# Kernel tuning notes

Hardware: AMD Instinct MI355X
Metric: run time of the kernel (lower is better)

The kernel has to match this reference:

```python
import jax, jax.numpy as jnp
import numpy as np
import math

HEAD_DIM = 64           # d_model // n_heads // 2
N_HEADS = 8
LAMBDA_INIT = 0.8 - 0.6 * math.exp(-0.3 * 6)  # depth=6
EPS = 1e-5


def setup_inputs() -> dict:
    key = jax.random.key(0)
    ks = jax.random.split(key, 8)
    B, T, S = 2, 2048, 2048
    return {
        "queries": jax.random.normal(ks[0], (B, 2 * N_HEADS, T, HEAD_DIM), jnp.float32),
        "keys": jax.random.normal(ks[1], (B, 2 * N_HEADS, S, HEAD_DIM), jnp.float32),
        "values": jax.random.normal(ks[2], (B, N_HEADS, S, 2 * HEAD_DIM), jnp.float32),
        "lambda_q1": 0.02 * jax.random.normal(ks[3], (HEAD_DIM,), jnp.float32),
        "lambda_k1": 0.02 * jax.random.normal(ks[4], (HEAD_DIM,), jnp.float32),
        "lambda_q2": 0.02 * jax.random.normal(ks[5], (HEAD_DIM,), jnp.float32),
        "lambda_k2": 0.02 * jax.random.normal(ks[6], (HEAD_DIM,), jnp.float32),
        "subln_weight": jnp.ones((2 * HEAD_DIM,), jnp.float32),
        "tgt_len": 2048,
        "src_len": 2048,
        "attn_mask": jnp.zeros((1,), jnp.bool_),
    }


def reference(queries, keys, values, lambda_q1, lambda_k1, lambda_q2, lambda_k2,
              subln_weight, tgt_len, src_len, attn_mask):
    B = queries.shape[0]
    scaling = HEAD_DIM ** -0.5
    q = queries * scaling
    # [B, 2H, T, S]
    attn_w = jnp.einsum('bhtd,bhsd->bhts', q, keys)
    attn_w = jax.nn.softmax(attn_w.astype(jnp.float32), axis=-1).astype(queries.dtype)
    lam1 = jnp.exp(jnp.sum(lambda_q1 * lambda_k1))
    lam2 = jnp.exp(jnp.sum(lambda_q2 * lambda_k2))
    lam_full = lam1 - lam2 + LAMBDA_INIT
    attn_w = attn_w.reshape(B, N_HEADS, 2, tgt_len, src_len)
    attn_w = attn_w[:, :, 0] - lam_full * attn_w[:, :, 1]   # [B, H, T, S]
    attn = jnp.einsum('bhts,bhse->bhte', attn_w, values)    # [B, H, T, 2*HEAD_DIM]
    # RMSNorm over last dim
    normed = attn * jax.lax.rsqrt(jnp.mean(jnp.square(attn.astype(jnp.float32)), axis=-1, keepdims=True) + EPS).astype(attn.dtype)
    normed = normed * subln_weight
    out = normed * (1.0 - LAMBDA_INIT)
    out = out.transpose(0, 2, 1, 3).reshape(B, tgt_len, N_HEADS * 2 * HEAD_DIM)
    return out
```

## Files before the change

### kernel.cpp

```cpp
#include <hip/hip_runtime.h>
#include <math.h>


#define NT    2048
#define D     64
#define DV    128
#define TQ    64
#define TS    32
#define NROUND (NT / (2 * TS))

#define LAMBDA_INIT 0.70082066706704814f
#define OUT_SCALE   0.29917933293295186f
#define QSCALE      0.18033688011112042f

typedef __attribute__((ext_vector_type(8)))  short    short8;
typedef __attribute__((ext_vector_type(4)))  short    short4v;
typedef __attribute__((ext_vector_type(8)))  _Float16 half8;
typedef __attribute__((ext_vector_type(2)))  __fp16   fp16x2;
typedef __attribute__((ext_vector_type(4)))  float    f32x4;
typedef unsigned short u16;
typedef unsigned int   u32;

#define MFMAH(a, b, c)  __builtin_amdgcn_mfma_f32_16x16x32_f16(a, b, c, 0, 0, 0)
#define MFMA16(a, b, c) __builtin_amdgcn_mfma_f32_16x16x32_bf16(a, b, c, 0, 0, 0)

#if __has_builtin(__builtin_amdgcn_exp2f)
#define EXP2F(x) __builtin_amdgcn_exp2f(x)
#else
#define EXP2F(x) exp2f(x)
#endif

union Hu { half8 v; _Float16 e[8]; u16 s[8]; short8 sv; };

__device__ __forceinline__ u16 f2h(float x) {
    Hu u; u.e[0] = (_Float16)x; return u.s[0];
}

__device__ __forceinline__ void glds16(const u16* g, const u16* l) {
    __builtin_amdgcn_global_load_lds(
        (const __attribute__((address_space(1))) void*)g,
        (__attribute__((address_space(3))) void*)l, 16, 0, 0);
}

__global__ __launch_bounds__(256) void prep_kv(
    const float* __restrict__ Kg, const float* __restrict__ Vg,
    const float* __restrict__ lq1, const float* __restrict__ lk1,
    const float* __restrict__ lq2, const float* __restrict__ lk2,
    u16* __restrict__ Kf, u16* __restrict__ Vf, float* __restrict__ lamw)
{
    __shared__ u16 th[64 * 136];
    const int bid = blockIdx.x;
    const int t   = threadIdx.x;
    if (bid < 2048) {
        const int idx = (bid * 256 + t) * 8;
        const float4 a = *(const float4*)(Kg + idx);
        const float4 b = *(const float4*)(Kg + idx + 4);
        Hu H;
        H.e[0] = (_Float16)a.x; H.e[1] = (_Float16)a.y;
        H.e[2] = (_Float16)a.z; H.e[3] = (_Float16)a.w;
        H.e[4] = (_Float16)b.x; H.e[5] = (_Float16)b.y;
        H.e[6] = (_Float16)b.z; H.e[7] = (_Float16)b.w;
        *(short8*)(Kf + idx) = H.sv;
        return;
    }
    if (bid == 2048) {
        if (t == 0) {
            float t1 = 0.f, t2 = 0.f;
            for (int i = 0; i < D; ++i) {
                t1 = fmaf(lq1[i], lk1[i], t1);
                t2 = fmaf(lq2[i], lk2[i], t2);
            }
            lamw[0] = __expf(t1) - __expf(t2) + LAMBDA_INIT;
        }
        return;
    }
    const int i  = bid - 2049;
    const int bh = i >> 5;
    const int eb = (i >> 4) & 1;
    const int sb = i & 15;
    const size_t vbase = (size_t)bh * NT * DV + (size_t)sb * 128 * DV + eb * 64;
    {
        const int r0 = t >> 4;
        const int c4 = (t & 15) * 4;
        #pragma unroll
        for (int rr = 0; rr < 8; ++rr) {
            const int row = r0 + rr * 16;
            const float4 x = *(const float4*)(Vg + vbase + (size_t)row * DV + c4);
            th[(c4 + 0) * 136 + row] = f2h(x.x);
            th[(c4 + 1) * 136 + row] = f2h(x.y);
            th[(c4 + 2) * 136 + row] = f2h(x.z);
            th[(c4 + 3) * 136 + row] = f2h(x.w);
        }
    }
    __syncthreads();
    const int e  = t >> 2;
    const int g  = t & 3;
    const size_t orow = ((size_t)bh * DV + eb * 64 + e) * NT + sb * 128;
    #pragma unroll
    for (int c = 0; c < 4; ++c) {
        Hu o;
        #pragma unroll
        for (int j = 0; j < 8; ++j)
            o.s[j] = th[e * 136 + g * 32 + 4 * c + (j & 3) + 16 * (j >> 2)];
        *(short8*)(Vf + orow + g * 32 + c * 8) = o.sv;
    }
}

struct SmemF {
    union {
        short8 c[4096];
        struct {
            float epi[2][32][132];
            float lbuf[2][2][2][32];
        } e;
    };
};

__global__ __launch_bounds__(512, 4) void diffattn_mfma17(
    const float* __restrict__ Qg,
    const u16* __restrict__ Kf, const u16* __restrict__ Vf,
    const float* __restrict__ lamw,
    const float* __restrict__ Wg, float* __restrict__ Outg)
{
    __shared__ SmemF sm;

    const int tid    = threadIdx.x;
    const int wv     = tid >> 6;
    const int lane   = tid & 63;
    const int quad   = lane >> 4;
    const int lc     = lane & 15;
    const int stripe = wv & 1;
    const int hh     = (wv >> 1) & 1;
    const int ks     = wv >> 2;
    const int wig    = wv & 3;
    const int qt     = blockIdx.x;
    const int bh     = blockIdx.y;
    const int b      = bh >> 3, h = bh & 7;

    const int head2b = b * 16 + 2 * h;
    const int bh8    = b * 8 + h;
    const float lam  = lamw[0];

    half8 qf[2][2];
    {
        const size_t qhead = (size_t)(head2b + hh) * NT * D;
        #pragma unroll
        for (int nq = 0; nq < 2; ++nq) {
            const int row = qt * TQ + stripe * 32 + nq * 16 + lc;
            #pragma unroll
            for (int k0 = 0; k0 < 2; ++k0) {
                const int d0 = k0 * 32 + quad * 8;
                const float4 x = *(const float4*)(Qg + qhead + (size_t)row * D + d0);
                const float4 y = *(const float4*)(Qg + qhead + (size_t)row * D + d0 + 4);
                Hu q;
                q.e[0] = (_Float16)(x.x * QSCALE); q.e[1] = (_Float16)(x.y * QSCALE);
                q.e[2] = (_Float16)(x.z * QSCALE); q.e[3] = (_Float16)(x.w * QSCALE);
                q.e[4] = (_Float16)(y.x * QSCALE); q.e[5] = (_Float16)(y.y * QSCALE);
                q.e[6] = (_Float16)(y.z * QSCALE); q.e[7] = (_Float16)(y.w * QSCALE);
                qf[nq][k0] = q.v;
            }
        }
    }

    f32x4 O_[2][8];
    #pragma unroll
    for (int nq = 0; nq < 2; ++nq)
        #pragma unroll
        for (int nt = 0; nt < 8; ++nt) O_[nq][nt] = (f32x4){0.f, 0.f, 0.f, 0.f};
    float lacA[2] = {0.f, 0.f};
    float lacB[2] = {0.f, 0.f};

    u32 kSrc[2], vSrc[2];
    u32 kLds[2], vLds[2];
    #pragma unroll
    for (int t = 0; t < 2; ++t) {
        const int p   = (wig * 2 + t) * 64 + lane;
        const int hhs = p >> 8;
        const int n   = (p >> 3) & 31;
        const int db  = (p & 7) ^ (n & 7);
        kSrc[t] = (u32)(((head2b + hhs) * NT + n) * D + db * 8);
        kLds[t] = (u32)((ks * 512 + (wig * 2 + t) * 64) * 16);
        const int e = p >> 2;
        const int u = (p & 3) ^ ((e >> 1) & 3);
        vSrc[t] = (u32)((bh8 * DV + e) * NT + u * 8);
        vLds[t] = (u32)((1024 + ks * 512 + (wig * 2 + t) * 64) * 16);
    }
    const u16* ldsu = (const u16*)&sm.c[0];

    #pragma unroll
    for (int t = 0; t < 2; ++t) {
        glds16(Kf + kSrc[t] + (u32)ks * (TS * D), ldsu + (kLds[t] >> 1));
        glds16(Vf + vSrc[t] + (u32)ks * TS,       ldsu + (vLds[t] >> 1));
    }
    __syncthreads();

    u32 kOff[2][2];
    #pragma unroll
    for (int k0 = 0; k0 < 2; ++k0)
        #pragma unroll
        for (int mt = 0; mt < 2; ++mt)
            kOff[k0][mt] = (u32)((ks * 512 + hh * 256 + (mt * 16 + lc) * 8 +
                                  ((4 * k0 + quad) ^ (lc & 7))) * 8);
    u32 vOff[8];
    {
        const int swzv = quad ^ ((lc >> 1) & 3);
        #pragma unroll
        for (int nt = 0; nt < 8; ++nt)
            vOff[nt] = (u32)((1024 + ks * 512 + (nt * 16 + lc) * 4 + swzv) * 8);
    }

    const f32x4 z4 = {0.f, 0.f, 0.f, 0.f};

    for (int r = 0; r < NROUND; ++r) {
        const u32 bo = ((u32)(r & 1)) << 14;

        if (r < NROUND - 1) {
            const u32 tn = (u32)(2 * (r + 1) + ks);
            const u32 ab = ((u32)((r + 1) & 1)) << 14;
            #pragma unroll
            for (int t = 0; t < 2; ++t) {
                glds16(Kf + kSrc[t] + tn * (TS * D), ldsu + ab + (kLds[t] >> 1));
                glds16(Vf + vSrc[t] + tn * TS,       ldsu + ab + (vLds[t] >> 1));
            }
        }

        f32x4 sf[2][2];
        {
            const half8 k00 = *(const half8*)(ldsu + bo + kOff[0][0]);
            const half8 k01 = *(const half8*)(ldsu + bo + kOff[0][1]);
            sf[0][0] = MFMAH(k00, qf[0][0], z4);
            sf[0][1] = MFMAH(k00, qf[1][0], z4);
            sf[1][0] = MFMAH(k01, qf[0][0], z4);
            sf[1][1] = MFMAH(k01, qf[1][0], z4);
            const half8 k10 = *(const half8*)(ldsu + bo + kOff[1][0]);
            const half8 k11 = *(const half8*)(ldsu + bo + kOff[1][1]);
            sf[0][0] = MFMAH(k10, qf[0][1], sf[0][0]);
            sf[0][1] = MFMAH(k10, qf[1][1], sf[0][1]);
            sf[1][0] = MFMAH(k11, qf[0][1], sf[1][0]);
            sf[1][1] = MFMAH(k11, qf[1][1], sf[1][1]);
        }

        half8 a8[2];
        #pragma unroll
        for (int nq = 0; nq < 2; ++nq) {
            union { half8 v; fp16x2 h[4]; } a;
            float lsA = lacA[nq], lsB = lacB[nq];
            const fp16x2 ones = {(__fp16)1.f, (__fp16)1.f};
            #pragma unroll
            for (int mt = 0; mt < 2; ++mt)
                #pragma unroll
                for (int ip = 0; ip < 2; ++ip) {
                    const float p0 = EXP2F(sf[mt][nq][2 * ip]);
                    const float p1 = EXP2F(sf[mt][nq][2 * ip + 1]);
                    const fp16x2 h2 = __builtin_amdgcn_cvt_pkrtz(p0, p1);
                    a.h[mt * 2 + ip] = h2;
                    if (((mt * 2 + ip) & 1) == 0)
                        lsA = __builtin_amdgcn_fdot2(h2, ones, lsA, false);
                    else
                        lsB = __builtin_amdgcn_fdot2(h2, ones, lsB, false);
                }
            lacA[nq] = lsA; lacB[nq] = lsB;
            a8[nq] = a.v;
        }

        #pragma unroll
        for (int nt = 0; nt < 8; ++nt) {
            const half8 vfr = *(const half8*)(ldsu + bo + vOff[nt]);
            #pragma unroll
            for (int nq = 0; nq < 2; ++nq)
                O_[nq][nt] = MFMAH(a8[nq], vfr, O_[nq][nt]);
        }

        __syncthreads();
    }

    {
        float s0 = lacA[0] + lacB[0];
        float s1 = lacA[1] + lacB[1];
        s0 += __shfl_xor(s0, 16); s0 += __shfl_xor(s0, 32);
        s1 += __shfl_xor(s1, 16); s1 += __shfl_xor(s1, 32);
        if (quad == 0) {
            sm.e.lbuf[hh][ks][stripe][lc]      = s0;
            sm.e.lbuf[hh][ks][stripe][16 + lc] = s1;
        }
    }
    __syncthreads();
    float coef[2][4];
    #pragma unroll
    for (int nq = 0; nq < 2; ++nq)
        #pragma unroll
        for (int i = 0; i < 4; ++i) {
            const int row = nq * 16 + quad * 4 + i;
            const float lt = sm.e.lbuf[hh][0][stripe][row] +
                             sm.e.lbuf[hh][1][stripe][row];
            coef[nq][i] = (hh == 0) ? (1.f / lt) : (-lam / lt);
        }
    __syncthreads();
    const int pid = hh * 2 + ks;
    #pragma unroll
    for (int p = 0; p < 4; ++p) {
        if (pid == p) {
            #pragma unroll
            for (int nq = 0; nq < 2; ++nq)
                #pragma unroll
                for (int i = 0; i < 4; ++i) {
                    const int row = nq * 16 + quad * 4 + i;
                    #pragma unroll
                    for (int nt = 0; nt < 8; ++nt) {
                        const int col = nt * 16 + lc;
                        const float v = O_[nq][nt][i] * coef[nq][i];
                        if (p == 0) sm.e.epi[stripe][row][col] = v;
                        else        sm.e.epi[stripe][row][col] += v;
                    }
                }
        }
        __syncthreads();
    }
    {
        const int r0 = wv * 8 + (lane >> 3);
        const int st = r0 >> 5, ri = r0 & 31;
        const int e0 = (lane & 7) * 16;
        float x[16];
        float ssq = 0.f;
        #pragma unroll
        for (int m = 0; m < 16; m += 4) {
            const float4 t4 = *(const float4*)&sm.e.epi[st][ri][e0 + m];
            x[m] = t4.x; x[m + 1] = t4.y; x[m + 2] = t4.z; x[m + 3] = t4.w;
            ssq += t4.x * t4.x + t4.y * t4.y + t4.z * t4.z + t4.w * t4.w;
        }
        ssq += __shfl_xor(ssq, 1);
        ssq += __shfl_xor(ssq, 2);
        ssq += __shfl_xor(ssq, 4);
        const float rsq = rsqrtf(ssq * (1.f / 128.f) + 1e-5f) * OUT_SCALE;
        const int rowg = qt * TQ + r0;
        const size_t base =
            ((size_t)b * NT + rowg) * (size_t)(8 * DV) + (size_t)h * DV;
        #pragma unroll
        for (int m = 0; m < 16; m += 4) {
            const float4 w4 = *(const float4*)(Wg + e0 + m);
            float4 o4;
            o4.x = x[m] * rsq * w4.x;
            o4.y = x[m + 1] * rsq * w4.y;
            o4.z = x[m + 2] * rsq * w4.z;
            o4.w = x[m + 3] * rsq * w4.w;
            *(float4*)(Outg + base + e0 + m) = o4;
        }
    }
}

__device__ __forceinline__ unsigned short f2bf(float x) {
    unsigned u = __float_as_uint(x);
    return (unsigned short)((u + 0x7fffu + ((u >> 16) & 1u)) >> 16);
}
__device__ __forceinline__ float bf2f(unsigned short h) {
    return __uint_as_float(((unsigned)h) << 16);
}

struct SmemB {
    union {
        struct {
            short8 kh[2][264];
            short8 kl[2][264];
            short8 vh[516];
            short8 vl[516];
            unsigned short ph[2][2560];
            unsigned short pl[2][2560];
        } L;
        float epi[2][32][132];
    };
};

__global__ __launch_bounds__(256, 2) void diffattn_fb(
    const float* __restrict__ Qg, const float* __restrict__ Kg,
    const float* __restrict__ Vg,
    const float* __restrict__ lq1, const float* __restrict__ lk1,
    const float* __restrict__ lq2, const float* __restrict__ lk2,
    const float* __restrict__ Wg, float* __restrict__ Outg)
{
    __shared__ SmemB sm;
    const int tid = threadIdx.x;
    const int wv = tid >> 6, lane = tid & 63;
    const int quad = lane >> 4, lc = lane & 15;
    const int stripe = wv & 1, hh = wv >> 1;
    const int qt = blockIdx.x, bh = blockIdx.y;
    const int b = bh >> 3, h = bh & 7;
    const size_t koff0 = ((size_t)(b * 16 + 2 * h)) * NT * D;
    const size_t voff  = ((size_t)(b * 8 + h)) * NT * DV;
    float t1 = 0.f, t2 = 0.f;
    for (int i = 0; i < D; ++i) {
        t1 = fmaf(lq1[i], lk1[i], t1);
        t2 = fmaf(lq2[i], lk2[i], t2);
    }
    const float lam = __expf(t1) - __expf(t2) + LAMBDA_INIT;
    short8 qfh[2][2], qfl[2][2];
    {
        const size_t qhead = ((size_t)(b * 16 + 2 * h + hh)) * NT * D;
        #pragma unroll
        for (int mt = 0; mt < 2; ++mt)
            #pragma unroll
            for (int k0 = 0; k0 < 2; ++k0) {
                const int row = qt * TQ + stripe * 32 + mt * 16 + lc;
                const int d0  = k0 * 32 + quad * 8;
                const float4 x = *(const float4*)(Qg + qhead + (size_t)row * D + d0);
                const float4 y = *(const float4*)(Qg + qhead + (size_t)row * D + d0 + 4);
                float f[8] = {x.x, x.y, x.z, x.w, y.x, y.y, y.z, y.w};
                #pragma unroll
                for (int j = 0; j < 8; ++j) {
                    const float v = f[j] * 0.125f;
                    const unsigned short hi = f2bf(v);
                    qfh[mt][k0][j] = (short)hi;
                    qfl[mt][k0][j] = (short)f2bf(v - bf2f(hi));
                }
            }
    }
    f32x4 O_[2][8];
    #pragma unroll
    for (int mt = 0; mt < 2; ++mt)
        #pragma unroll
        for (int nt = 0; nt < 8; ++nt) O_[mt][nt] = (f32x4){0.f, 0.f, 0.f, 0.f};
    float m_[2][4], l_[2][4], a_[2][4];
    #pragma unroll
    for (int mt = 0; mt < 2; ++mt)
        #pragma unroll
        for (int i = 0; i < 4; ++i) { m_[mt][i] = -1e30f; l_[mt][i] = 0.f; }
    const int s_hh = tid >> 7;
    const int s_n  = (tid >> 2) & 31;
    const int s_d0 = (tid & 3) * 16;
    const int s_e0 = tid & 31;
    const int s_s0 = ((tid >> 5) & 7) * 4;
    const int s_sb = s_s0 >> 3;
    const int s_hs = (s_s0 & 4) ? 1 : 0;
    for (int kt = 0; kt < NT / TS; ++kt) {
        const int kb = kt * TS;
        __syncthreads();
        {
            const float* kp = Kg + koff0 + (size_t)s_hh * NT * D +
                              (size_t)(kb + s_n) * D + s_d0;
            const float4 x0 = ((const float4*)kp)[0];
            const float4 x1 = ((const float4*)kp)[1];
            const float4 x2 = ((const float4*)kp)[2];
            const float4 x3 = ((const float4*)kp)[3];
            float f[16] = {x0.x, x0.y, x0.z, x0.w, x1.x, x1.y, x1.z, x1.w,
                           x2.x, x2.y, x2.z, x2.w, x3.x, x3.y, x3.z, x3.w};
            short8 c0h, c0l, c1h, c1l;
            #pragma unroll
            for (int j = 0; j < 8; ++j) {
                unsigned short hi = f2bf(f[j]);
                c0h[j] = (short)hi; c0l[j] = (short)f2bf(f[j] - bf2f(hi));
                hi = f2bf(f[8 + j]);
                c1h[j] = (short)hi; c1l[j] = (short)f2bf(f[8 + j] - bf2f(hi));
            }
            const int db0 = s_d0 >> 3;
            sm.L.kh[s_hh][db0 * 33 + s_n]       = c0h;
            sm.L.kl[s_hh][db0 * 33 + s_n]       = c0l;
            sm.L.kh[s_hh][(db0 + 1) * 33 + s_n] = c1h;
            sm.L.kl[s_hh][(db0 + 1) * 33 + s_n] = c1l;
        }
        {
            #pragma unroll
            for (int j = 0; j < 4; ++j) {
                const int e = s_e0 + 32 * j;
                float f[4];
                #pragma unroll
                for (int i = 0; i < 4; ++i)
                    f[i] = Vg[voff + (size_t)(kb + s_s0 + i) * DV + e];
                short4v hi4, lo4;
                #pragma unroll
                for (int i = 0; i < 4; ++i) {
                    const unsigned short hi = f2bf(f[i]);
                    hi4[i] = (short)hi;
                    lo4[i] = (short)f2bf(f[i] - bf2f(hi));
                }
                ((short4v*)&sm.L.vh[s_sb * 129 + e])[s_hs] = hi4;
                ((short4v*)&sm.L.vl[s_sb * 129 + e])[s_hs] = lo4;
            }
        }
        __syncthreads();
        f32x4 s_f[2][2];
        #pragma unroll
        for (int mt = 0; mt < 2; ++mt)
            #pragma unroll
            for (int nt = 0; nt < 2; ++nt) s_f[mt][nt] = (f32x4){0.f, 0.f, 0.f, 0.f};
        #pragma unroll
        for (int k0 = 0; k0 < 2; ++k0)
            #pragma unroll
            for (int nt = 0; nt < 2; ++nt) {
                const short8 kh = sm.L.kh[hh][(4 * k0 + quad) * 33 + nt * 16 + lc];
                const short8 kl = sm.L.kl[hh][(4 * k0 + quad) * 33 + nt * 16 + lc];
                #pragma unroll
                for (int mt = 0; mt < 2; ++mt) {
                    s_f[mt][nt] = MFMA16(qfh[mt][k0], kh, s_f[mt][nt]);
                    s_f[mt][nt] = MFMA16(qfl[mt][k0], kh, s_f[mt][nt]);
                    s_f[mt][nt] = MFMA16(qfh[mt][k0], kl, s_f[mt][nt]);
                }
            }
        #pragma unroll
        for (int mt = 0; mt < 2; ++mt)
            #pragma unroll
            for (int i = 0; i < 4; ++i) {
                const float v0 = s_f[mt][0][i], v1 = s_f[mt][1][i];
                float mx = fmaxf(v0, v1);
                mx = fmaxf(mx, __shfl_xor(mx, 1));
                mx = fmaxf(mx, __shfl_xor(mx, 2));
                mx = fmaxf(mx, __shfl_xor(mx, 4));
                mx = fmaxf(mx, __shfl_xor(mx, 8));
                const float mn = fmaxf(m_[mt][i], mx);
                const float al = __expf(m_[mt][i] - mn);
                const float p0 = __expf(v0 - mn);
                const float p1 = __expf(v1 - mn);
                float rs = p0 + p1;
                rs += __shfl_xor(rs, 1);
                rs += __shfl_xor(rs, 2);
                rs += __shfl_xor(rs, 4);
                rs += __shfl_xor(rs, 8);
                l_[mt][i] = l_[mt][i] * al + rs;
                m_[mt][i] = mn;
                a_[mt][i] = al;
                const int r = stripe * 32 + mt * 16 + quad * 4 + i;
                const unsigned short h0 = f2bf(p0);
                sm.L.ph[hh][r * 40 + lc]      = h0;
                sm.L.pl[hh][r * 40 + lc]      = f2bf(p0 - bf2f(h0));
                const unsigned short h1 = f2bf(p1);
                sm.L.ph[hh][r * 40 + 16 + lc] = h1;
                sm.L.pl[hh][r * 40 + 16 + lc] = f2bf(p1 - bf2f(h1));
            }
        __syncthreads();
        #pragma unroll
        for (int mt = 0; mt < 2; ++mt)
            #pragma unroll
            for (int nt = 0; nt < 8; ++nt)
                #pragma unroll
                for (int i = 0; i < 4; ++i) O_[mt][nt][i] *= a_[mt][i];
        short8 pah[2], pal[2];
        #pragma unroll
        for (int mt = 0; mt < 2; ++mt) {
            const int r = stripe * 32 + mt * 16 + lc;
            pah[mt] = *(const short8*)&sm.L.ph[hh][r * 40 + quad * 8];
            pal[mt] = *(const short8*)&sm.L.pl[hh][r * 40 + quad * 8];
        }
        #pragma unroll
        for (int nt = 0; nt < 8; ++nt) {
            const short8 vh = sm.L.vh[quad * 129 + nt * 16 + lc];
            const short8 vl = sm.L.vl[quad * 129 + nt * 16 + lc];
            #pragma unroll
            for (int mt = 0; mt < 2; ++mt) {
                O_[mt][nt] = MFMA16(pah[mt], vh, O_[mt][nt]);
                O_[mt][nt] = MFMA16(pal[mt], vh, O_[mt][nt]);
                O_[mt][nt] = MFMA16(pah[mt], vl, O_[mt][nt]);
            }
        }
    }
    __syncthreads();
    if (hh == 1) {
        #pragma unroll
        for (int mt = 0; mt < 2; ++mt)
            #pragma unroll
            for (int i = 0; i < 4; ++i) {
                const float inv = lam / l_[mt][i];
                const int r = mt * 16 + quad * 4 + i;
                #pragma unroll
                for (int nt = 0; nt < 8; ++nt)
                    sm.epi[stripe][r][nt * 16 + lc] = O_[mt][nt][i] * inv;
            }
    }
    __syncthreads();
    if (hh == 0) {
        float wvv[8];
        #pragma unroll
        for (int nt = 0; nt < 8; ++nt) wvv[nt] = Wg[nt * 16 + lc];
        #pragma unroll
        for (int mt = 0; mt < 2; ++mt)
            #pragma unroll
            for (int i = 0; i < 4; ++i) {
                const float inv1 = 1.f / l_[mt][i];
                const int r = mt * 16 + quad * 4 + i;
                float od[8];
                float ss = 0.f;
                #pragma unroll
                for (int nt = 0; nt < 8; ++nt) {
                    od[nt] = O_[mt][nt][i] * inv1 - sm.epi[stripe][r][nt * 16 + lc];
                    ss = fmaf(od[nt], od[nt], ss);
                }
                ss += __shfl_xor(ss, 1);
                ss += __shfl_xor(ss, 2);
                ss += __shfl_xor(ss, 4);
                ss += __shfl_xor(ss, 8);
                const float rsq = rsqrtf(ss * (1.f / 128.f) + 1e-5f) * OUT_SCALE;
                const int rowg = qt * TQ + stripe * 32 + r;
                const size_t base =
                    ((size_t)b * NT + rowg) * (size_t)(8 * DV) + (size_t)h * DV;
                #pragma unroll
                for (int nt = 0; nt < 8; ++nt)
                    Outg[base + nt * 16 + lc] = od[nt] * rsq * wvv[nt];
            }
    }
}

extern "C" void kernel_launch(void* const* d_in, const int* in_sizes, int n_in,
                              void* d_out, int out_size, void* d_ws, size_t ws_size,
                              hipStream_t stream) {
    const float* Q   = (const float*)d_in[0];
    const float* K   = (const float*)d_in[1];
    const float* V   = (const float*)d_in[2];
    const float* lq1 = (const float*)d_in[3];
    const float* lk1 = (const float*)d_in[4];
    const float* lq2 = (const float*)d_in[5];
    const float* lk2 = (const float*)d_in[6];
    const float* W   = (const float*)d_in[7];
    float* Out = (float*)d_out;
    const size_t NEED = 2ull * 4194304ull * sizeof(u16) + 16;
    if (ws_size >= NEED) {
        u16*   Kf   = (u16*)d_ws;
        u16*   Vf   = Kf + 4194304;
        float* lamw = (float*)(Vf + 4194304);
        prep_kv<<<2561, 256, 0, stream>>>(K, V, lq1, lk1, lq2, lk2, Kf, Vf, lamw);
        diffattn_mfma17<<<dim3(NT / TQ, 16), 512, 0, stream>>>(
            Q, Kf, Vf, lamw, W, Out);
    } else {
        diffattn_fb<<<dim3(NT / TQ, 16), 256, 0, stream>>>(
            Q, K, V, lq1, lk1, lq2, lk2, W, Out);
    }
}
```

Before: 169.3 us.

## Shrink query tile to 32 rows and drop split-KV within block

```diff
diff --git a/kernel.cpp b/kernel.cpp
--- a/kernel.cpp
+++ b/kernel.cpp
@@ -5,9 +5,9 @@
 #define NT    2048
 #define D     64
 #define DV    128
-#define TQ    64
+#define TQB   32
 #define TS    32
-#define NROUND (NT / (2 * TS))
+#define NROUND (NT / TS)
 
 #define LAMBDA_INIT 0.70082066706704814f
 #define OUT_SCALE   0.29917933293295186f
@@ -108,15 +108,12 @@
 
 struct SmemF {
     union {
-        short8 c[4096];
-        struct {
-            float epi[2][32][132];
-            float lbuf[2][2][2][32];
-        } e;
+        short8 c[2048];
+        float  epi[32][132];
     };
 };
 
-__global__ __launch_bounds__(512, 4) void diffattn_mfma17(
+__global__ __launch_bounds__(256, 4) void diffattn_mfma18(
     const float* __restrict__ Qg,
     const u16* __restrict__ Kf, const u16* __restrict__ Vf,
     const float* __restrict__ lamw,
@@ -124,73 +121,65 @@
 {
     __shared__ SmemF sm;
 
-    const int tid    = threadIdx.x;
-    const int wv     = tid >> 6;
-    const int lane   = tid & 63;
-    const int quad   = lane >> 4;
-    const int lc     = lane & 15;
-    const int stripe = wv & 1;
-    const int hh     = (wv >> 1) & 1;
-    const int ks     = wv >> 2;
-    const int wig    = wv & 3;
-    const int qt     = blockIdx.x;
-    const int bh     = blockIdx.y;
-    const int b      = bh >> 3, h = bh & 7;
+    const int tid  = threadIdx.x;
+    const int wv   = tid >> 6;
+    const int lane = tid & 63;
+    const int quad = lane >> 4;
+    const int lc   = lane & 15;
+    const int hh   = wv & 1;
+    const int qs   = wv >> 1;
+    const int qt   = blockIdx.x;
+    const int bh   = blockIdx.y;
+    const int b    = bh >> 3, h = bh & 7;
 
     const int head2b = b * 16 + 2 * h;
     const int bh8    = b * 8 + h;
     const float lam  = lamw[0];
 
-    half8 qf[2][2];
+    half8 qf[2];
     {
         const size_t qhead = (size_t)(head2b + hh) * NT * D;
-        #pragma unroll
-        for (int nq = 0; nq < 2; ++nq) {
-            const int row = qt * TQ + stripe * 32 + nq * 16 + lc;
-            #pragma unroll
-            for (int k0 = 0; k0 < 2; ++k0) {
-                const int d0 = k0 * 32 + quad * 8;
-                const float4 x = *(const float4*)(Qg + qhead + (size_t)row * D + d0);
-                const float4 y = *(const float4*)(Qg + qhead + (size_t)row * D + d0 + 4);
-                Hu q;
-                q.e[0] = (_Float16)(x.x * QSCALE); q.e[1] = (_Float16)(x.y * QSCALE);
-                q.e[2] = (_Float16)(x.z * QSCALE); q.e[3] = (_Float16)(x.w * QSCALE);
-                q.e[4] = (_Float16)(y.x * QSCALE); q.e[5] = (_Float16)(y.y * QSCALE);
-                q.e[6] = (_Float16)(y.z * QSCALE); q.e[7] = (_Float16)(y.w * QSCALE);
-                qf[nq][k0] = q.v;
-            }
-        }
-    }
-
-    f32x4 O_[2][8];
-    #pragma unroll
-    for (int nq = 0; nq < 2; ++nq)
-        #pragma unroll
-        for (int nt = 0; nt < 8; ++nt) O_[nq][nt] = (f32x4){0.f, 0.f, 0.f, 0.f};
-    float lacA[2] = {0.f, 0.f};
-    float lacB[2] = {0.f, 0.f};
+        const int row = qt * TQB + qs * 16 + lc;
+        #pragma unroll
+        for (int k0 = 0; k0 < 2; ++k0) {
+            const int d0 = k0 * 32 + quad * 8;
+            const float4 x = *(const float4*)(Qg + qhead + (size_t)row * D + d0);
+            const float4 y = *(const float4*)(Qg + qhead + (size_t)row * D + d0 + 4);
+            Hu q;
+            q.e[0] = (_Float16)(x.x * QSCALE); q.e[1] = (_Float16)(x.y * QSCALE);
+            q.e[2] = (_Float16)(x.z * QSCALE); q.e[3] = (_Float16)(x.w * QSCALE);
+            q.e[4] = (_Float16)(y.x * QSCALE); q.e[5] = (_Float16)(y.y * QSCALE);
+            q.e[6] = (_Float16)(y.z * QSCALE); q.e[7] = (_Float16)(y.w * QSCALE);
+            qf[k0] = q.v;
+        }
+    }
+
+    f32x4 O_[8];
+    #pragma unroll
+    for (int nt = 0; nt < 8; ++nt) O_[nt] = (f32x4){0.f, 0.f, 0.f, 0.f};
+    float lacA = 0.f, lacB = 0.f;
 
     u32 kSrc[2], vSrc[2];
-    u32 kLds[2], vLds[2];
+    u32 kDst[2], vDst[2];
     #pragma unroll
     for (int t = 0; t < 2; ++t) {
-        const int p   = (wig * 2 + t) * 64 + lane;
+        const int p   = (wv * 2 + t) * 64 + lane;
         const int hhs = p >> 8;
         const int n   = (p >> 3) & 31;
         const int db  = (p & 7) ^ (n & 7);
         kSrc[t] = (u32)(((head2b + hhs) * NT + n) * D + db * 8);
-        kLds[t] = (u32)((ks * 512 + (wig * 2 + t) * 64) * 16);
+        kDst[t] = (u32)(((wv * 2 + t) * 64) * 8);
         const int e = p >> 2;
         const int u = (p & 3) ^ ((e >> 1) & 3);
         vSrc[t] = (u32)((bh8 * DV + e) * NT + u * 8);
-        vLds[t] = (u32)((1024 + ks * 512 + (wig * 2 + t) * 64) * 16);
+        vDst[t] = (u32)(4096 + ((wv * 2 + t) * 64) * 8);
     }
     const u16* ldsu = (const u16*)&sm.c[0];
 
     #pragma unroll
     for (int t = 0; t < 2; ++t) {
-        glds16(Kf + kSrc[t] + (u32)ks * (TS * D), ldsu + (kLds[t] >> 1));
-        glds16(Vf + vSrc[t] + (u32)ks * TS,       ldsu + (vLds[t] >> 1));
+        glds16(Kf + kSrc[t], ldsu + kDst[t]);
+        glds16(Vf + vSrc[t], ldsu + vDst[t]);
     }
     __syncthreads();
 
@@ -199,132 +188,109 @@
     for (int k0 = 0; k0 < 2; ++k0)
         #pragma unroll
         for (int mt = 0; mt < 2; ++mt)
-            kOff[k0][mt] = (u32)((ks * 512 + hh * 256 + (mt * 16 + lc) * 8 +
+            kOff[k0][mt] = (u32)((hh * 256 + (mt * 16 + lc) * 8 +
                                   ((4 * k0 + quad) ^ (lc & 7))) * 8);
     u32 vOff[8];
     {
         const int swzv = quad ^ ((lc >> 1) & 3);
         #pragma unroll
         for (int nt = 0; nt < 8; ++nt)
-            vOff[nt] = (u32)((1024 + ks * 512 + (nt * 16 + lc) * 4 + swzv) * 8);
+            vOff[nt] = (u32)(4096 + ((nt * 16 + lc) * 4 + swzv) * 8);
     }
 
     const f32x4 z4 = {0.f, 0.f, 0.f, 0.f};
 
     for (int r = 0; r < NROUND; ++r) {
-        const u32 bo = ((u32)(r & 1)) << 14;
+        const u32 bo = ((u32)(r & 1)) << 13;
 
         if (r < NROUND - 1) {
-            const u32 tn = (u32)(2 * (r + 1) + ks);
-            const u32 ab = ((u32)((r + 1) & 1)) << 14;
+            const u32 tn = (u32)(r + 1);
+            const u32 ab = ((u32)((r + 1) & 1)) << 13;
             #pragma unroll
             for (int t = 0; t < 2; ++t) {
-                glds16(Kf + kSrc[t] + tn * (TS * D), ldsu + ab + (kLds[t] >> 1));
-                glds16(Vf + vSrc[t] + tn * TS,       ldsu + ab + (vLds[t] >> 1));
-            }
-        }
-
-        f32x4 sf[2][2];
+                glds16(Kf + kSrc[t] + tn * (TS * D), ldsu + ab + kDst[t]);
+                glds16(Vf + vSrc[t] + tn * TS,       ldsu + ab + vDst[t]);
+            }
+        }
+
+        f32x4 sf[2];
         {
             const half8 k00 = *(const half8*)(ldsu + bo + kOff[0][0]);
             const half8 k01 = *(const half8*)(ldsu + bo + kOff[0][1]);
-            sf[0][0] = MFMAH(k00, qf[0][0], z4);
-            sf[0][1] = MFMAH(k00, qf[1][0], z4);
-            sf[1][0] = MFMAH(k01, qf[0][0], z4);
-            sf[1][1] = MFMAH(k01, qf[1][0], z4);
+            sf[0] = MFMAH(k00, qf[0], z4);
+            sf[1] = MFMAH(k01, qf[0], z4);
             const half8 k10 = *(const half8*)(ldsu + bo + kOff[1][0]);
             const half8 k11 = *(const half8*)(ldsu + bo + kOff[1][1]);
-            sf[0][0] = MFMAH(k10, qf[0][1], sf[0][0]);
-            sf[0][1] = MFMAH(k10, qf[1][1], sf[0][1]);
-            sf[1][0] = MFMAH(k11, qf[0][1], sf[1][0]);
-            sf[1][1] = MFMAH(k11, qf[1][1], sf[1][1]);
-        }
-
-        half8 a8[2];
-        #pragma unroll
-        for (int nq = 0; nq < 2; ++nq) {
-            union { half8 v; fp16x2 h[4]; } a;
-            float lsA = lacA[nq], lsB = lacB[nq];
+            sf[0] = MFMAH(k10, qf[1], sf[0]);
+            sf[1] = MFMAH(k11, qf[1], sf[1]);
+        }
+
+        union { half8 v; fp16x2 h[4]; } a;
+        {
             const fp16x2 ones = {(__fp16)1.f, (__fp16)1.f};
             #pragma unroll
             for (int mt = 0; mt < 2; ++mt)
                 #pragma unroll
                 for (int ip = 0; ip < 2; ++ip) {
-                    const float p0 = EXP2F(sf[mt][nq][2 * ip]);
-                    const float p1 = EXP2F(sf[mt][nq][2 * ip + 1]);
+                    const float p0 = EXP2F(sf[mt][2 * ip]);
+                    const float p1 = EXP2F(sf[mt][2 * ip + 1]);
                     const fp16x2 h2 = __builtin_amdgcn_cvt_pkrtz(p0, p1);
                     a.h[mt * 2 + ip] = h2;
                     if (((mt * 2 + ip) & 1) == 0)
-                        lsA = __builtin_amdgcn_fdot2(h2, ones, lsA, false);
+                        lacA = __builtin_amdgcn_fdot2(h2, ones, lacA, false);
                     else
-                        lsB = __builtin_amdgcn_fdot2(h2, ones, lsB, false);
+                        lacB = __builtin_amdgcn_fdot2(h2, ones, lacB, false);
                 }
-            lacA[nq] = lsA; lacB[nq] = lsB;
-            a8[nq] = a.v;
         }
 
         #pragma unroll
         for (int nt = 0; nt < 8; ++nt) {
             const half8 vfr = *(const half8*)(ldsu + bo + vOff[nt]);
-            #pragma unroll
-            for (int nq = 0; nq < 2; ++nq)
-                O_[nq][nt] = MFMAH(a8[nq], vfr, O_[nq][nt]);
+            O_[nt] = MFMAH(a.v, vfr, O_[nt]);
         }
 
         __syncthreads();
     }
 
+    float coef[4];
     {
-        float s0 = lacA[0] + lacB[0];
-        float s1 = lacA[1] + lacB[1];
-        s0 += __shfl_xor(s0, 16); s0 += __shfl_xor(s0, 32);
-        s1 += __shfl_xor(s1, 16); s1 += __shfl_xor(s1, 32);
-        if (quad == 0) {
-            sm.e.lbuf[hh][ks][stripe][lc]      = s0;
-            sm.e.lbuf[hh][ks][stripe][16 + lc] = s1;
+        float s0 = lacA + lacB;
+        s0 += __shfl_xor(s0, 16);
+        s0 += __shfl_xor(s0, 32);
+        #pragma unroll
+        for (int i = 0; i < 4; ++i) {
+            const float li = __shfl(s0, quad * 4 + i);
+            coef[i] = (hh == 0) ? (1.f / li) : (-lam / li);
+        }
+    }
+    if (hh == 0) {
+        #pragma unroll
+        for (int i = 0; i < 4; ++i) {
+            const int row = qs * 16 + quad * 4 + i;
+            #pragma unroll
+            for (int nt = 0; nt < 8; ++nt)
+                sm.epi[row][nt * 16 + lc] = O_[nt][i] * coef[i];
         }
     }
     __syncthreads();
-    float coef[2][4];
-    #pragma unroll
-    for (int nq = 0; nq < 2; ++nq)
+    if (hh == 1) {
         #pragma unroll
         for (int i = 0; i < 4; ++i) {
-            const int row = nq * 16 + quad * 4 + i;
-            const float lt = sm.e.lbuf[hh][0][stripe][row] +
-                             sm.e.lbuf[hh][1][stripe][row];
-            coef[nq][i] = (hh == 0) ? (1.f / lt) : (-lam / lt);
-        }
+            const int row = qs * 16 + quad * 4 + i;
+            #pragma unroll
+            for (int nt = 0; nt < 8; ++nt)
+                sm.epi[row][nt * 16 + lc] += O_[nt][i] * coef[i];
+        }
+    }
     __syncthreads();
-    const int pid = hh * 2 + ks;
-    #pragma unroll
-    for (int p = 0; p < 4; ++p) {
-        if (pid == p) {
-            #pragma unroll
-            for (int nq = 0; nq < 2; ++nq)
-                #pragma unroll
-                for (int i = 0; i < 4; ++i) {
-                    const int row = nq * 16 + quad * 4 + i;
-                    #pragma unroll
-                    for (int nt = 0; nt < 8; ++nt) {
-                        const int col = nt * 16 + lc;
-                        const float v = O_[nq][nt][i] * coef[nq][i];
-                        if (p == 0) sm.e.epi[stripe][row][col] = v;
-                        else        sm.e.epi[stripe][row][col] += v;
-                    }
-                }
-        }
-        __syncthreads();
-    }
     {
-        const int r0 = wv * 8 + (lane >> 3);
-        const int st = r0 >> 5, ri = r0 & 31;
-        const int e0 = (lane & 7) * 16;
+        const int ri = tid >> 3;
+        const int e0 = (tid & 7) * 16;
         float x[16];
         float ssq = 0.f;
         #pragma unroll
         for (int m = 0; m < 16; m += 4) {
-            const float4 t4 = *(const float4*)&sm.e.epi[st][ri][e0 + m];
+            const float4 t4 = *(const float4*)&sm.epi[ri][e0 + m];
             x[m] = t4.x; x[m + 1] = t4.y; x[m + 2] = t4.z; x[m + 3] = t4.w;
             ssq += t4.x * t4.x + t4.y * t4.y + t4.z * t4.z + t4.w * t4.w;
         }
@@ -332,7 +298,7 @@
         ssq += __shfl_xor(ssq, 2);
         ssq += __shfl_xor(ssq, 4);
         const float rsq = rsqrtf(ssq * (1.f / 128.f) + 1e-5f) * OUT_SCALE;
-        const int rowg = qt * TQ + r0;
+        const int rowg = qt * TQB + ri;
         const size_t base =
             ((size_t)b * NT + rowg) * (size_t)(8 * DV) + (size_t)h * DV;
         #pragma unroll
@@ -399,7 +365,7 @@
         for (int mt = 0; mt < 2; ++mt)
             #pragma unroll
             for (int k0 = 0; k0 < 2; ++k0) {
-                const int row = qt * TQ + stripe * 32 + mt * 16 + lc;
+                const int row = qt * 64 + stripe * 32 + mt * 16 + lc;
                 const int d0  = k0 * 32 + quad * 8;
                 const float4 x = *(const float4*)(Qg + qhead + (size_t)row * D + d0);
                 const float4 y = *(const float4*)(Qg + qhead + (size_t)row * D + d0 + 4);
@@ -586,7 +552,7 @@
                 ss += __shfl_xor(ss, 4);
                 ss += __shfl_xor(ss, 8);
                 const float rsq = rsqrtf(ss * (1.f / 128.f) + 1e-5f) * OUT_SCALE;
-                const int rowg = qt * TQ + stripe * 32 + r;
+                const int rowg = qt * 64 + stripe * 32 + r;
                 const size_t base =
                     ((size_t)b * NT + rowg) * (size_t)(8 * DV) + (size_t)h * DV;
                 #pragma unroll
@@ -614,10 +580,10 @@
         u16*   Vf   = Kf + 4194304;
         float* lamw = (float*)(Vf + 4194304);
         prep_kv<<<2561, 256, 0, stream>>>(K, V, lq1, lk1, lq2, lk2, Kf, Vf, lamw);
-        diffattn_mfma17<<<dim3(NT / TQ, 16), 512, 0, stream>>>(
+        diffattn_mfma18<<<dim3(NT / TQB, 16), 256, 0, stream>>>(
             Q, Kf, Vf, lamw, W, Out);
     } else {
-        diffattn_fb<<<dim3(NT / TQ, 16), 256, 0, stream>>>(
+        diffattn_fb<<<dim3(NT / 64, 16), 256, 0, stream>>>(
             Q, K, V, lq1, lk1, lq2, lk2, W, Out);
     }
 }
```

Result: slower. 183.3 us (+8.2%).

## Give each wave all 64 query rows, halving block to 256 threads

Applied to the files above, without the earlier changes.

```diff
diff --git a/kernel.cpp b/kernel.cpp
--- a/kernel.cpp
+++ b/kernel.cpp
@@ -110,13 +110,13 @@
     union {
         short8 c[4096];
         struct {
-            float epi[2][32][132];
-            float lbuf[2][2][2][32];
+            float epi[64][132];
+            float lbuf[2][2][64];
         } e;
     };
 };
 
-__global__ __launch_bounds__(512, 4) void diffattn_mfma17(
+__global__ __launch_bounds__(256, 2) void diffattn_mfma19(
     const float* __restrict__ Qg,
     const u16* __restrict__ Kf, const u16* __restrict__ Vf,
     const float* __restrict__ lamw,
@@ -124,29 +124,27 @@
 {
     __shared__ SmemF sm;
 
-    const int tid    = threadIdx.x;
-    const int wv     = tid >> 6;
-    const int lane   = tid & 63;
-    const int quad   = lane >> 4;
-    const int lc     = lane & 15;
-    const int stripe = wv & 1;
-    const int hh     = (wv >> 1) & 1;
-    const int ks     = wv >> 2;
-    const int wig    = wv & 3;
-    const int qt     = blockIdx.x;
-    const int bh     = blockIdx.y;
-    const int b      = bh >> 3, h = bh & 7;
+    const int tid  = threadIdx.x;
+    const int wv   = tid >> 6;
+    const int lane = tid & 63;
+    const int quad = lane >> 4;
+    const int lc   = lane & 15;
+    const int hh   = wv & 1;
+    const int ks   = wv >> 1;
+    const int qt   = blockIdx.x;
+    const int bh   = blockIdx.y;
+    const int b    = bh >> 3, h = bh & 7;
 
     const int head2b = b * 16 + 2 * h;
     const int bh8    = b * 8 + h;
     const float lam  = lamw[0];
 
-    half8 qf[2][2];
+    half8 qf[4][2];
     {
         const size_t qhead = (size_t)(head2b + hh) * NT * D;
         #pragma unroll
-        for (int nq = 0; nq < 2; ++nq) {
-            const int row = qt * TQ + stripe * 32 + nq * 16 + lc;
+        for (int nq = 0; nq < 4; ++nq) {
+            const int row = qt * TQ + nq * 16 + lc;
             #pragma unroll
             for (int k0 = 0; k0 < 2; ++k0) {
                 const int d0 = k0 * 32 + quad * 8;
@@ -162,35 +160,35 @@
         }
     }
 
-    f32x4 O_[2][8];
-    #pragma unroll
-    for (int nq = 0; nq < 2; ++nq)
+    f32x4 O_[4][8];
+    #pragma unroll
+    for (int nq = 0; nq < 4; ++nq)
         #pragma unroll
         for (int nt = 0; nt < 8; ++nt) O_[nq][nt] = (f32x4){0.f, 0.f, 0.f, 0.f};
-    float lacA[2] = {0.f, 0.f};
-    float lacB[2] = {0.f, 0.f};
-
-    u32 kSrc[2], vSrc[2];
-    u32 kLds[2], vLds[2];
-    #pragma unroll
-    for (int t = 0; t < 2; ++t) {
-        const int p   = (wig * 2 + t) * 64 + lane;
+    float lacA[4] = {0.f, 0.f, 0.f, 0.f};
+    float lacB[4] = {0.f, 0.f, 0.f, 0.f};
+
+    u32 kSrc[4], vSrc[4];
+    u32 kDst[4], vDst[4];
+    #pragma unroll
+    for (int t = 0; t < 4; ++t) {
+        const int p   = hh * 256 + t * 64 + lane;
         const int hhs = p >> 8;
         const int n   = (p >> 3) & 31;
         const int db  = (p & 7) ^ (n & 7);
         kSrc[t] = (u32)(((head2b + hhs) * NT + n) * D + db * 8);
-        kLds[t] = (u32)((ks * 512 + (wig * 2 + t) * 64) * 16);
+        kDst[t] = (u32)((ks * 512 + hh * 256 + t * 64) * 8);
         const int e = p >> 2;
         const int u = (p & 3) ^ ((e >> 1) & 3);
         vSrc[t] = (u32)((bh8 * DV + e) * NT + u * 8);
-        vLds[t] = (u32)((1024 + ks * 512 + (wig * 2 + t) * 64) * 16);
+        vDst[t] = (u32)((1024 + ks * 512 + hh * 256 + t * 64) * 8);
     }
     const u16* ldsu = (const u16*)&sm.c[0];
 
     #pragma unroll
-    for (int t = 0; t < 2; ++t) {
-        glds16(Kf + kSrc[t] + (u32)ks * (TS * D), ldsu + (kLds[t] >> 1));
-        glds16(Vf + vSrc[t] + (u32)ks * TS,       ldsu + (vLds[t] >> 1));
+    for (int t = 0; t < 4; ++t) {
+        glds16(Kf + kSrc[t] + (u32)ks * (TS * D), ldsu + kDst[t]);
+        glds16(Vf + vSrc[t] + (u32)ks * TS,       ldsu + vDst[t]);
     }
     __syncthreads();
 
@@ -218,31 +216,33 @@
             const u32 tn = (u32)(2 * (r + 1) + ks);
             const u32 ab = ((u32)((r + 1) & 1)) << 14;
             #pragma unroll
-            for (int t = 0; t < 2; ++t) {
-                glds16(Kf + kSrc[t] + tn * (TS * D), ldsu + ab + (kLds[t] >> 1));
-                glds16(Vf + vSrc[t] + tn * TS,       ldsu + ab + (vLds[t] >> 1));
-            }
-        }
-
-        f32x4 sf[2][2];
+            for (int t = 0; t < 4; ++t) {
+                glds16(Kf + kSrc[t] + tn * (TS * D), ldsu + ab + kDst[t]);
+                glds16(Vf + vSrc[t] + tn * TS,       ldsu + ab + vDst[t]);
+            }
+        }
+
+        f32x4 sf[2][4];
         {
             const half8 k00 = *(const half8*)(ldsu + bo + kOff[0][0]);
             const half8 k01 = *(const half8*)(ldsu + bo + kOff[0][1]);
-            sf[0][0] = MFMAH(k00, qf[0][0], z4);
-            sf[0][1] = MFMAH(k00, qf[1][0], z4);
-            sf[1][0] = MFMAH(k01, qf[0][0], z4);
-            sf[1][1] = MFMAH(k01, qf[1][0], z4);
+            #pragma unroll
+            for (int nq = 0; nq < 4; ++nq) {
+                sf[0][nq] = MFMAH(k00, qf[nq][0], z4);
+                sf[1][nq] = MFMAH(k01, qf[nq][0], z4);
+            }
             const half8 k10 = *(const half8*)(ldsu + bo + kOff[1][0]);
             const half8 k11 = *(const half8*)(ldsu + bo + kOff[1][1]);
-            sf[0][0] = MFMAH(k10, qf[0][1], sf[0][0]);
-            sf[0][1] = MFMAH(k10, qf[1][1], sf[0][1]);
-            sf[1][0] = MFMAH(k11, qf[0][1], sf[1][0]);
-            sf[1][1] = MFMAH(k11, qf[1][1], sf[1][1]);
-        }
-
-        half8 a8[2];
-        #pragma unroll
-        for (int nq = 0; nq < 2; ++nq) {
+            #pragma unroll
+            for (int nq = 0; nq < 4; ++nq) {
+                sf[0][nq] = MFMAH(k10, qf[nq][1], sf[0][nq]);
+                sf[1][nq] = MFMAH(k11, qf[nq][1], sf[1][nq]);
+            }
+        }
+
+        half8 a8[4];
+        #pragma unroll
+        for (int nq = 0; nq < 4; ++nq) {
             union { half8 v; fp16x2 h[4]; } a;
             float lsA = lacA[nq], lsB = lacB[nq];
             const fp16x2 ones = {(__fp16)1.f, (__fp16)1.f};
@@ -267,7 +267,7 @@
         for (int nt = 0; nt < 8; ++nt) {
             const half8 vfr = *(const half8*)(ldsu + bo + vOff[nt]);
             #pragma unroll
-            for (int nq = 0; nq < 2; ++nq)
+            for (int nq = 0; nq < 4; ++nq)
                 O_[nq][nt] = MFMAH(a8[nq], vfr, O_[nq][nt]);
         }
 
@@ -275,24 +275,22 @@
     }
 
     {
-        float s0 = lacA[0] + lacB[0];
-        float s1 = lacA[1] + lacB[1];
-        s0 += __shfl_xor(s0, 16); s0 += __shfl_xor(s0, 32);
-        s1 += __shfl_xor(s1, 16); s1 += __shfl_xor(s1, 32);
-        if (quad == 0) {
-            sm.e.lbuf[hh][ks][stripe][lc]      = s0;
-            sm.e.lbuf[hh][ks][stripe][16 + lc] = s1;
+        #pragma unroll
+        for (int nq = 0; nq < 4; ++nq) {
+            float s = lacA[nq] + lacB[nq];
+            s += __shfl_xor(s, 16);
+            s += __shfl_xor(s, 32);
+            if (quad == 0) sm.e.lbuf[hh][ks][nq * 16 + lc] = s;
         }
     }
     __syncthreads();
-    float coef[2][4];
-    #pragma unroll
-    for (int nq = 0; nq < 2; ++nq)
+    float coef[4][4];
+    #pragma unroll
+    for (int nq = 0; nq < 4; ++nq)
         #pragma unroll
         for (int i = 0; i < 4; ++i) {
             const int row = nq * 16 + quad * 4 + i;
-            const float lt = sm.e.lbuf[hh][0][stripe][row] +
-                             sm.e.lbuf[hh][1][stripe][row];
+            const float lt = sm.e.lbuf[hh][0][row] + sm.e.lbuf[hh][1][row];
             coef[nq][i] = (hh == 0) ? (1.f / lt) : (-lam / lt);
         }
     __syncthreads();
@@ -301,7 +299,7 @@
     for (int p = 0; p < 4; ++p) {
         if (pid == p) {
             #pragma unroll
-            for (int nq = 0; nq < 2; ++nq)
+            for (int nq = 0; nq < 4; ++nq)
                 #pragma unroll
                 for (int i = 0; i < 4; ++i) {
                     const int row = nq * 16 + quad * 4 + i;
@@ -309,34 +307,32 @@
                     for (int nt = 0; nt < 8; ++nt) {
                         const int col = nt * 16 + lc;
                         const float v = O_[nq][nt][i] * coef[nq][i];
-                        if (p == 0) sm.e.epi[stripe][row][col] = v;
-                        else        sm.e.epi[stripe][row][col] += v;
+                        if (p == 0) sm.e.epi[row][col] = v;
+                        else        sm.e.epi[row][col] += v;
                     }
                 }
         }
         __syncthreads();
     }
     {
-        const int r0 = wv * 8 + (lane >> 3);
-        const int st = r0 >> 5, ri = r0 & 31;
-        const int e0 = (lane & 7) * 16;
-        float x[16];
+        const int ri = tid >> 2;
+        const int e0 = (tid & 3) * 32;
+        float x[32];
         float ssq = 0.f;
         #pragma unroll
-        for (int m = 0; m < 16; m += 4) {
-            const float4 t4 = *(const float4*)&sm.e.epi[st][ri][e0 + m];
+        for (int m = 0; m < 32; m += 4) {
+            const float4 t4 = *(const float4*)&sm.e.epi[ri][e0 + m];
             x[m] = t4.x; x[m + 1] = t4.y; x[m + 2] = t4.z; x[m + 3] = t4.w;
             ssq += t4.x * t4.x + t4.y * t4.y + t4.z * t4.z + t4.w * t4.w;
         }
         ssq += __shfl_xor(ssq, 1);
         ssq += __shfl_xor(ssq, 2);
-        ssq += __shfl_xor(ssq, 4);
         const float rsq = rsqrtf(ssq * (1.f / 128.f) + 1e-5f) * OUT_SCALE;
-        const int rowg = qt * TQ + r0;
+        const int rowg = qt * TQ + ri;
         const size_t base =
             ((size_t)b * NT + rowg) * (size_t)(8 * DV) + (size_t)h * DV;
         #pragma unroll
-        for (int m = 0; m < 16; m += 4) {
+        for (int m = 0; m < 32; m += 4) {
             const float4 w4 = *(const float4*)(Wg + e0 + m);
             float4 o4;
             o4.x = x[m] * rsq * w4.x;
@@ -399,7 +395,7 @@
         for (int mt = 0; mt < 2; ++mt)
             #pragma unroll
             for (int k0 = 0; k0 < 2; ++k0) {
-                const int row = qt * TQ + stripe * 32 + mt * 16 + lc;
+                const int row = qt * 64 + stripe * 32 + mt * 16 + lc;
                 const int d0  = k0 * 32 + quad * 8;
                 const float4 x = *(const float4*)(Qg + qhead + (size_t)row * D + d0);
                 const float4 y = *(const float4*)(Qg + qhead + (size_t)row * D + d0 + 4);
@@ -586,7 +582,7 @@
                 ss += __shfl_xor(ss, 4);
                 ss += __shfl_xor(ss, 8);
                 const float rsq = rsqrtf(ss * (1.f / 128.f) + 1e-5f) * OUT_SCALE;
-                const int rowg = qt * TQ + stripe * 32 + r;
+                const int rowg = qt * 64 + stripe * 32 + r;
                 const size_t base =
                     ((size_t)b * NT + rowg) * (size_t)(8 * DV) + (size_t)h * DV;
                 #pragma unroll
@@ -614,10 +610,10 @@
         u16*   Vf   = Kf + 4194304;
         float* lamw = (float*)(Vf + 4194304);
         prep_kv<<<2561, 256, 0, stream>>>(K, V, lq1, lk1, lq2, lk2, Kf, Vf, lamw);
-        diffattn_mfma17<<<dim3(NT / TQ, 16), 512, 0, stream>>>(
+        diffattn_mfma19<<<dim3(NT / TQ, 16), 256, 0, stream>>>(
             Q, Kf, Vf, lamw, W, Out);
     } else {
-        diffattn_fb<<<dim3(NT / TQ, 16), 256, 0, stream>>>(
+        diffattn_fb<<<dim3(NT / 64, 16), 256, 0, stream>>>(
             Q, K, V, lq1, lk1, lq2, lk2, W, Out);
     }
 }
```

Result: no change. 170.9 us (+0.9%).
